# Kernel tuning notes

Hardware: AMD Instinct MI355X
Metric: run time of the kernel (lower is better)

## Reference

```python
import jax, jax.numpy as jnp
import numpy as np

NUM_USERS = 50000
NUM_ITEMS = 50000
N_NODES = NUM_USERS + NUM_ITEMS
NNZ = 3200000
EMB_DIM = 64
N_LAYERS = 3
BATCH = 16384


def setup_inputs() -> dict:
    key = jax.random.key(0)
    ks = jax.random.split(key, 7)
    user_emb = 0.1 * jax.random.normal(ks[0], (NUM_USERS, EMB_DIM), dtype=jnp.float32)
    item_emb = 0.1 * jax.random.normal(ks[1], (NUM_ITEMS, EMB_DIM), dtype=jnp.float32)
    edge_val = jax.random.uniform(ks[2], (NNZ,), dtype=jnp.float32)
    edge_src = jax.random.randint(ks[3], (NNZ,), 0, N_NODES, dtype=jnp.int32)
    edge_dst = jax.random.randint(ks[4], (NNZ,), 0, N_NODES, dtype=jnp.int32)
    users = jax.random.randint(ks[5], (BATCH,), 0, NUM_USERS, dtype=jnp.int32)
    items = jax.random.randint(ks[6], (BATCH,), 0, NUM_ITEMS, dtype=jnp.int32)
    return {"user_emb": user_emb, "item_emb": item_emb, "edge_val": edge_val,
            "edge_src": edge_src, "edge_dst": edge_dst, "users": users, "items": items}


def _computer(user_emb, item_emb, edge_val, edge_src, edge_dst):
    # LightGCN propagation: all_emb <- A @ all_emb, mean over layer outputs (incl. layer 0)
    all_emb = jnp.concatenate([user_emb, item_emb], axis=0)  # [N, D]
    acc = all_emb
    for _ in range(N_LAYERS):
        msg = edge_val[:, None] * all_emb[edge_src]          # [nnz, D]
        all_emb = jax.ops.segment_sum(msg, edge_dst, num_segments=N_NODES)
        acc = acc + all_emb
    light_out = acc / jnp.float32(N_LAYERS + 1)
    return light_out[:NUM_USERS], light_out[NUM_USERS:]


def reference(user_emb, item_emb, edge_val, edge_src, edge_dst, users, items):
    all_users, all_items = _computer(user_emb, item_emb, edge_val, edge_src, edge_dst)
    users_emb = all_users[users]                              # [B, D]
    items_emb = all_items[items]                              # [B, D]
    gamma = jnp.sum(users_emb * items_emb, axis=1)            # [B]
    return gamma
```

## Files before the change

### kernel.cpp

```cpp
#include <hip/hip_runtime.h>

#define NUM_USERS 50000
#define NUM_ITEMS 50000
#define N_NODES   100000
#define NNZ       3200000
#define EMB_DIM   64
#define N_LAYERS  3
#define BATCH     16384

#define NBUCK 512
#define ABITS 8
#define NODES_PER_BUCK 256
#define TILE_EDGES 8192
#define NBUCK_USED ((N_NODES + NODES_PER_BUCK - 1) / NODES_PER_BUCK)
#define CAP 9472
#define NCELL 1024

typedef unsigned long long ull;
typedef float v2f __attribute__((ext_vector_type(2)));

__device__ inline unsigned bf16pair(float a, float b) {
    unsigned ua = __float_as_uint(a), ub = __float_as_uint(b);
    unsigned r0 = (ua + 0x7fffu + ((ua >> 16) & 1u)) >> 16;
    unsigned r1 = (ub + 0x7fffu + ((ub >> 16) & 1u)) >> 16;
    return r0 | (r1 << 16);
}
__device__ inline float blo(unsigned u) { return __uint_as_float(u << 16); }
__device__ inline float bhi(unsigned u) { return __uint_as_float(u & 0xffff0000u); }

__device__ inline void pkfma(v2f& d, v2f a, v2f b) {
    asm("v_pk_fma_f32 %0, %1, %2, %0" : "+v"(d) : "v"(a), "v"(b));
}

__device__ inline void accP(v2f& sA, v2f& sB, v2f& sC, v2f& sD, uint4 g, unsigned r) {
    float w = (float)(r >> 17);
    v2f w2 = {w, w};
    v2f e0 = {blo(g.x), bhi(g.x)};
    v2f e1 = {blo(g.y), bhi(g.y)};
    v2f e2 = {blo(g.z), bhi(g.z)};
    v2f e3 = {blo(g.w), bhi(g.w)};
    pkfma(sA, e0, w2);
    pkfma(sB, e1, w2);
    pkfma(sC, e2, w2);
    pkfma(sD, e3, w2);
}

__device__ inline uint4 gath(const unsigned char* __restrict__ base, unsigned r, unsigned dOff) {
    unsigned off = ((r & 0x1FFFFu) << 7) + dOff;
    return *(const uint4*)(base + off);
}

__device__ inline void roundU(const unsigned char* __restrict__ A16,
                              const unsigned* __restrict__ p, unsigned dOff,
                              v2f& sA, v2f& sB, v2f& sC, v2f& sD) {
    uint4 R = *(const uint4*)p;
    uint4 g0 = gath(A16, R.x, dOff);
    uint4 g1 = gath(A16, R.y, dOff);
    uint4 g2 = gath(A16, R.z, dOff);
    uint4 g3 = gath(A16, R.w, dOff);
    accP(sA, sB, sC, sD, g0, R.x);
    accP(sA, sB, sC, sD, g1, R.y);
    accP(sA, sB, sC, sD, g2, R.z);
    accP(sA, sB, sC, sD, g3, R.w);
}

__device__ inline void pull_pair(const unsigned char* __restrict__ A16,
                                 uint4* __restrict__ B16,
                                 const unsigned* __restrict__ sorted,
                                 const int* __restrict__ rowStart,
                                 const int* __restrict__ deg,
                                 int nA, int nB, int d8, unsigned dOff) {
    int dA = deg[nA], dB = deg[nB];
    const unsigned* pA = sorted + rowStart[nA];
    const unsigned* pB = sorted + rowStart[nB];

    v2f s00 = {0.f,0.f}, s01 = {0.f,0.f}, s02 = {0.f,0.f}, s03 = {0.f,0.f};
    v2f s10 = {0.f,0.f}, s11 = {0.f,0.f}, s12 = {0.f,0.f}, s13 = {0.f,0.f};

    #pragma unroll
    for (int base = 0; base < 48; base += 4) {
        if (dA > base) roundU(A16, pA + base, dOff, s00, s01, s02, s03);
        if (dB > base) roundU(A16, pB + base, dOff, s10, s11, s12, s13);
    }
    if (__builtin_expect((dA > 48) || (dB > 48), 0)) {
        for (int base = 48; base < dA; base += 4)
            roundU(A16, pA + base, dOff, s00, s01, s02, s03);
        for (int base = 48; base < dB; base += 4)
            roundU(A16, pB + base, dOff, s10, s11, s12, s13);
    }

    const float k15 = 1.f / 32768.f;
    uint4 h;
    h.x = bf16pair(s00.x * k15, s00.y * k15);
    h.y = bf16pair(s01.x * k15, s01.y * k15);
    h.z = bf16pair(s02.x * k15, s02.y * k15);
    h.w = bf16pair(s03.x * k15, s03.y * k15);
    B16[(((long long)nA) << 3) + d8] = h;
    h.x = bf16pair(s10.x * k15, s10.y * k15);
    h.y = bf16pair(s11.x * k15, s11.y * k15);
    h.z = bf16pair(s12.x * k15, s12.y * k15);
    h.w = bf16pair(s13.x * k15, s13.y * k15);
    B16[(((long long)nB) << 3) + d8] = h;
}

__global__ void init_emb_kernel(const float* __restrict__ ue,
                                const float* __restrict__ ie,
                                unsigned* __restrict__ E0,
                                int* __restrict__ bucketCursor) {
    int idx = blockIdx.x * blockDim.x + threadIdx.x;
    if (blockIdx.x == 0 && threadIdx.x < 256) {
        bucketCursor[threadIdx.x]       = threadIdx.x * CAP;
        bucketCursor[threadIdx.x + 256] = (threadIdx.x + 256) * CAP;
    }
    const int total = N_NODES * (EMB_DIM / 4);
    if (idx >= total) return;
    const int uoff = NUM_USERS * (EMB_DIM / 4);
    float4 v;
    if (idx < uoff) v = ((const float4*)ue)[idx];
    else            v = ((const float4*)ie)[idx - uoff];
    uint2 h;
    h.x = bf16pair(v.x, v.y);
    h.y = bf16pair(v.z, v.w);
    ((uint2*)E0)[idx] = h;
}

__global__ void partA_kernel(const float* __restrict__ ev,
                             const int*  __restrict__ es,
                             const int*  __restrict__ ed,
                             int* __restrict__ bucketCursor,
                             ull* __restrict__ tmp) {
    __shared__ int hist[NBUCK];
    __shared__ int base[NBUCK];
    __shared__ int cnt2[NBUCK];
    int tid = threadIdx.x;
    int e0 = blockIdx.x * TILE_EDGES;

    int      mySrc[8], myDst[8];
    unsigned myQ[8];

    for (int i = tid; i < NBUCK; i += 1024) hist[i] = 0;
    __syncthreads();

    #pragma unroll
    for (int k = 0; k < 8; ++k) {
        int e = e0 + k * 1024 + tid;
        if (e < NNZ) {
            mySrc[k] = es[e];
            myDst[k] = ed[e];
            myQ[k]   = (unsigned)fminf(ev[e] * 32768.f + 0.5f, 32767.f);
            atomicAdd(&hist[((unsigned)myDst[k]) >> ABITS], 1);
        } else {
            myDst[k] = -1;
        }
    }
    __syncthreads();

    for (int i = tid; i < NBUCK; i += 1024) {
        int c = hist[i];
        base[i] = c ? atomicAdd(&bucketCursor[i], c) : 0;
        cnt2[i] = 0;
    }
    __syncthreads();

    #pragma unroll
    for (int k = 0; k < 8; ++k) {
        int dst = myDst[k];
        if (dst < 0) continue;
        int b = ((unsigned)dst) >> ABITS;
        int pos = base[b] + atomicAdd(&cnt2[b], 1);
        if (pos < (b + 1) * CAP) {
            ull rec = (ull)(unsigned)(mySrc[k] | ((dst & (NODES_PER_BUCK - 1)) << 17))
                    | ((ull)myQ[k] << 25);
            tmp[pos] = rec;
        }
    }
}

__global__ void partB_kernel(const ull* __restrict__ tmp,
                             const int* __restrict__ bucketCursor,
                             int* __restrict__ rowStart,
                             int* __restrict__ deg,
                             unsigned* __restrict__ sorted) {
    __shared__ int cnt[NCELL];
    __shared__ int nsc[NODES_PER_BUCK];
    __shared__ int nstart[NODES_PER_BUCK];
    __shared__ int cur[NCELL];
    int b = blockIdx.x;
    int tid = threadIdx.x;
    int nodeLo = b << ABITS;
    int startE = b * CAP;
    int endE   = bucketCursor[b];

    cnt[tid] = 0;
    __syncthreads();

    ull myRec[9];
    int myCell[9];
    int nRec = 0;
    #pragma unroll
    for (int k = 0; k < 9; ++k) {
        int i = startE + k * 1024 + tid;
        if (i < endE) {
            myRec[k] = tmp[i];
            nRec = k + 1;
            unsigned src = (unsigned)(myRec[k] & 0x1FFFFULL);
            int q = (int)(src >> 15); if (q > 3) q = 3;
            int dl = (int)((myRec[k] >> 17) & (NODES_PER_BUCK - 1));
            myCell[k] = (dl << 2) + q;
            atomicAdd(&cnt[myCell[k]], 1);
        }
    }
    __syncthreads();

    int p4 = 0;
    if (tid < NODES_PER_BUCK) {
        int tot = cnt[tid*4] + cnt[tid*4+1] + cnt[tid*4+2] + cnt[tid*4+3];
        p4 = (tot + 3) & ~3;
        nsc[tid] = p4;
    }
    __syncthreads();
    for (int o = 1; o < NODES_PER_BUCK; o <<= 1) {
        int add = 0;
        if (tid < NODES_PER_BUCK && tid >= o) add = nsc[tid - o];
        __syncthreads();
        if (tid < NODES_PER_BUCK) nsc[tid] += add;
        __syncthreads();
    }
    if (tid < NODES_PER_BUCK) {
        int ns = startE + nsc[tid] - p4;
        nstart[tid] = ns;
        int node = nodeLo + tid;
        if (node < N_NODES) {
            rowStart[node] = ns;
            deg[node] = p4;
        }
    }
    __syncthreads();

    {
        int n = tid >> 2, q = tid & 3;
        int c = nstart[n];
        if (q > 0) c += cnt[n*4];
        if (q > 1) c += cnt[n*4+1];
        if (q > 2) c += cnt[n*4+2];
        cur[tid] = c;
    }
    __syncthreads();

    for (int k = 0; k < nRec; ++k) {
        ull rec = myRec[k];
        unsigned o = (unsigned)(rec & 0x1FFFFULL) | ((unsigned)((rec >> 25) & 0x7FFF) << 17);
        int pos = atomicAdd(&cur[myCell[k]], 1);
        if (pos < startE + CAP) sorted[pos] = o;
    }
    __syncthreads();

    if (tid < NODES_PER_BUCK) {
        int tot = cnt[tid*4] + cnt[tid*4+1] + cnt[tid*4+2] + cnt[tid*4+3];
        int end = nstart[tid] + ((tot + 3) & ~3);
        for (int p = nstart[tid] + tot; p < end; ++p)
            if (p < startE + CAP) sorted[p] = 0;
    }
}

__global__ void __launch_bounds__(256, 6)
pull_sync_kernel(const unsigned char* __restrict__ A16,
                 uint4* __restrict__ B16,
                 const unsigned* __restrict__ sorted,
                 const int* __restrict__ rowStart,
                 const int* __restrict__ deg) {
    int wid = (blockIdx.x << 2) + (threadIdx.x >> 6);
    if (wid >= N_NODES / 16) return;
    int lane = threadIdx.x & 63;
    int eg = lane >> 3;
    int d8 = lane & 7;
    unsigned dOff = (unsigned)d8 << 4;
    int nA = (wid << 4) + (eg << 1);
    pull_pair(A16, B16, sorted, rowStart, deg, nA, nA + 1, d8, dOff);
}

__global__ void __launch_bounds__(256, 6)
pull_gated_kernel(const unsigned char* __restrict__ A16,
                  uint4* __restrict__ B16,
                  const unsigned* __restrict__ sorted,
                  const int* __restrict__ rowStart,
                  const int* __restrict__ deg,
                  const int* __restrict__ users,
                  const int* __restrict__ items) {
    int wid = (blockIdx.x << 2) + (threadIdx.x >> 6);
    if (wid >= (2 * BATCH) / 16) return;
    int lane = threadIdx.x & 63;
    int eg = lane >> 3;
    int d8 = lane & 7;
    unsigned dOff = (unsigned)d8 << 4;
    int e = (wid << 4) + (eg << 1);
    int nA = (e     < BATCH) ? users[e]     : NUM_USERS + items[e - BATCH];
    int nB = (e + 1 < BATCH) ? users[e + 1] : NUM_USERS + items[e + 1 - BATCH];
    pull_pair(A16, B16, sorted, rowStart, deg, nA, nB, d8, dOff);
}

__global__ void dot_kernel(const unsigned* __restrict__ E0,
                           const unsigned* __restrict__ B1,
                           const unsigned* __restrict__ B2,
                           const unsigned* __restrict__ B3,
                           const int* __restrict__ users,
                           const int* __restrict__ items,
                           float* __restrict__ out) {
    int t = blockIdx.x * blockDim.x + threadIdx.x;
    int b = t >> 5;
    int lane = t & 31;
    if (b >= BATCH) return;
    long long uo = ((long long)users[b] << 5) + lane;
    long long io = ((long long)(items[b] + NUM_USERS) << 5) + lane;
    unsigned a0 = E0[uo], a1 = B1[uo], a2 = B2[uo], a3 = B3[uo];
    unsigned c0 = E0[io], c1 = B1[io], c2 = B2[io], c3 = B3[io];
    float ux = (blo(a0) + blo(a1)) + (blo(a2) + blo(a3));
    float uy = (bhi(a0) + bhi(a1)) + (bhi(a2) + bhi(a3));
    float ix = (blo(c0) + blo(c1)) + (blo(c2) + blo(c3));
    float iy = (bhi(c0) + bhi(c1)) + (bhi(c2) + bhi(c3));
    float p = ux * ix + uy * iy;
    #pragma unroll
    for (int off = 16; off >= 1; off >>= 1)
        p += __shfl_xor(p, off, 64);
    if (lane == 0) out[b] = p * 0.0625f;
}

extern "C" void kernel_launch(void* const* d_in, const int* in_sizes, int n_in,
                              void* d_out, int out_size, void* d_ws, size_t ws_size,
                              hipStream_t stream) {
    const float* user_emb = (const float*)d_in[0];
    const float* item_emb = (const float*)d_in[1];
    const float* edge_val = (const float*)d_in[2];
    const int*   edge_src = (const int*)d_in[3];
    const int*   edge_dst = (const int*)d_in[4];
    const int*   users    = (const int*)d_in[5];
    const int*   items    = (const int*)d_in[6];
    float* out = (float*)d_out;

    const size_t emb16Bytes = (size_t)N_NODES * EMB_DIM * 2;
    const size_t sortBytes  = (size_t)NBUCK_USED * CAP * sizeof(unsigned);
    const size_t tmpBytes   = (size_t)NBUCK_USED * CAP * sizeof(ull);
    const size_t nodeBytes  = (size_t)N_NODES * sizeof(int);

    char* w = (char*)d_ws;
    unsigned* E0           = (unsigned*)(w); w += emb16Bytes;
    unsigned* B1           = (unsigned*)(w); w += emb16Bytes;
    unsigned* B2           = (unsigned*)(w); w += emb16Bytes;
    unsigned* B3           = (unsigned*)(w); w += emb16Bytes;
    unsigned* sorted       = (unsigned*)(w); w += sortBytes;
    ull*      tmp          = (ull*)(w);      w += tmpBytes;
    int*      deg          = (int*)(w);      w += nodeBytes;
    int*      rowStart     = (int*)(w);      w += nodeBytes;
    int*      bucketCursor = (int*)(w);      w += NBUCK * sizeof(int);

    const int vecTotal   = N_NODES * (EMB_DIM / 4);
    const int initBlocks = (vecTotal + 255) / 256;
    const int tileBlocks = (NNZ + TILE_EDGES - 1) / TILE_EDGES;

    init_emb_kernel<<<initBlocks, 256, 0, stream>>>(user_emb, item_emb, E0, bucketCursor);

    partA_kernel<<<tileBlocks, 1024, 0, stream>>>(edge_val, edge_src, edge_dst,
                                                  bucketCursor, tmp);
    partB_kernel<<<NBUCK_USED, 1024, 0, stream>>>(tmp, bucketCursor,
                                                  rowStart, deg, sorted);

    const int syncBlocks = (N_NODES / 16 + 3) / 4;
    pull_sync_kernel<<<syncBlocks, 256, 0, stream>>>((const unsigned char*)E0, (uint4*)B1,
                                                     sorted, rowStart, deg);
    pull_sync_kernel<<<syncBlocks, 256, 0, stream>>>((const unsigned char*)B1, (uint4*)B2,
                                                     sorted, rowStart, deg);

    const int gatedBlocks = ((2 * BATCH) / 16 + 3) / 4;
    pull_gated_kernel<<<gatedBlocks, 256, 0, stream>>>((const unsigned char*)B2, (uint4*)B3,
                                                       sorted, rowStart, deg, users, items);

    const int dotBlocks = (BATCH * 32 + 255) / 256;
    dot_kernel<<<dotBlocks, 256, 0, stream>>>(E0, B1, B2, B3, users, items, out);
}
```

Baseline: 296.0 us.

## Assign one wavefront per node in pull kernels with cross-lane reduction

Each pull kernel now gives a whole 64-lane wavefront to a single destination node instead of 16 nodes per wavefront (two per 8-lane group). The 8 edge groups split that node's edge list, and the partial sums are combined with xor shuffles before one group writes the bf16 row. Edge indices are read and results written with nontemporal hints. The aim is better load balance and more memory-level parallelism across the ~32 edges per node, at the cost of shuffle reductions, padding tails, and 8x more wavefronts.

Measured after the change: 279.5 us. 1.06x faster.

```diff
diff --git a/kernel.cpp b/kernel.cpp
--- a/kernel.cpp
+++ b/kernel.cpp
@@ -18,6 +18,7 @@
 
 typedef unsigned long long ull;
 typedef float v2f __attribute__((ext_vector_type(2)));
+typedef unsigned v4u __attribute__((ext_vector_type(4)));
 
 __device__ inline unsigned bf16pair(float a, float b) {
     unsigned ua = __float_as_uint(a), ub = __float_as_uint(b);
@@ -30,6 +31,9 @@
 
 __device__ inline void pkfma(v2f& d, v2f a, v2f b) {
     asm("v_pk_fma_f32 %0, %1, %2, %0" : "+v"(d) : "v"(a), "v"(b));
+}
+__device__ inline void pkadd(v2f& d, v2f a) {
+    asm("v_pk_add_f32 %0, %1, %0" : "+v"(d) : "v"(a));
 }
 
 __device__ inline void accP(v2f& sA, v2f& sB, v2f& sC, v2f& sD, uint4 g, unsigned r) {
@@ -50,57 +54,71 @@
     return *(const uint4*)(base + off);
 }
 
-__device__ inline void roundU(const unsigned char* __restrict__ A16,
-                              const unsigned* __restrict__ p, unsigned dOff,
-                              v2f& sA, v2f& sB, v2f& sC, v2f& sD) {
-    uint4 R = *(const uint4*)p;
-    uint4 g0 = gath(A16, R.x, dOff);
-    uint4 g1 = gath(A16, R.y, dOff);
-    uint4 g2 = gath(A16, R.z, dOff);
-    uint4 g3 = gath(A16, R.w, dOff);
-    accP(sA, sB, sC, sD, g0, R.x);
-    accP(sA, sB, sC, sD, g1, R.y);
-    accP(sA, sB, sC, sD, g2, R.z);
-    accP(sA, sB, sC, sD, g3, R.w);
-}
-
-__device__ inline void pull_pair(const unsigned char* __restrict__ A16,
-                                 uint4* __restrict__ B16,
+__device__ inline unsigned ntl(const unsigned* __restrict__ p) {
+    return __builtin_nontemporal_load(p);
+}
+
+__device__ inline void wred(v2f& s) {
+    v2f t;
+    t.x = __shfl_xor(s.x, 8, 64);  t.y = __shfl_xor(s.y, 8, 64);  pkadd(s, t);
+    t.x = __shfl_xor(s.x, 16, 64); t.y = __shfl_xor(s.y, 16, 64); pkadd(s, t);
+    t.x = __shfl_xor(s.x, 32, 64); t.y = __shfl_xor(s.y, 32, 64); pkadd(s, t);
+}
+
+__device__ inline void pull_node(const unsigned char* __restrict__ A16,
+                                 unsigned* __restrict__ B16,
                                  const unsigned* __restrict__ sorted,
-                                 const int* __restrict__ rowStart,
-                                 const int* __restrict__ deg,
-                                 int nA, int nB, int d8, unsigned dOff) {
-    int dA = deg[nA], dB = deg[nB];
-    const unsigned* pA = sorted + rowStart[nA];
-    const unsigned* pB = sorted + rowStart[nB];
-
-    v2f s00 = {0.f,0.f}, s01 = {0.f,0.f}, s02 = {0.f,0.f}, s03 = {0.f,0.f};
-    v2f s10 = {0.f,0.f}, s11 = {0.f,0.f}, s12 = {0.f,0.f}, s13 = {0.f,0.f};
-
-    #pragma unroll
-    for (int base = 0; base < 48; base += 4) {
-        if (dA > base) roundU(A16, pA + base, dOff, s00, s01, s02, s03);
-        if (dB > base) roundU(A16, pB + base, dOff, s10, s11, s12, s13);
-    }
-    if (__builtin_expect((dA > 48) || (dB > 48), 0)) {
-        for (int base = 48; base < dA; base += 4)
-            roundU(A16, pA + base, dOff, s00, s01, s02, s03);
-        for (int base = 48; base < dB; base += 4)
-            roundU(A16, pB + base, dOff, s10, s11, s12, s13);
-    }
-
-    const float k15 = 1.f / 32768.f;
-    uint4 h;
-    h.x = bf16pair(s00.x * k15, s00.y * k15);
-    h.y = bf16pair(s01.x * k15, s01.y * k15);
-    h.z = bf16pair(s02.x * k15, s02.y * k15);
-    h.w = bf16pair(s03.x * k15, s03.y * k15);
-    B16[(((long long)nA) << 3) + d8] = h;
-    h.x = bf16pair(s10.x * k15, s10.y * k15);
-    h.y = bf16pair(s11.x * k15, s11.y * k15);
-    h.z = bf16pair(s12.x * k15, s12.y * k15);
-    h.w = bf16pair(s13.x * k15, s13.y * k15);
-    B16[(((long long)nB) << 3) + d8] = h;
+                                 int node, int start, int cnt, int lane) {
+    int eg = lane >> 3;
+    int d8 = lane & 7;
+    unsigned dOff = (unsigned)d8 << 4;
+    const unsigned* ep = sorted + start;
+
+    v2f sA = {0.f,0.f}, sB = {0.f,0.f}, sC = {0.f,0.f}, sD = {0.f,0.f};
+    int j = 0;
+    while (j + 32 <= cnt) {
+        unsigned r0 = ntl(ep + j + eg),      r1 = ntl(ep + j + 8 + eg);
+        unsigned r2 = ntl(ep + j + 16 + eg), r3 = ntl(ep + j + 24 + eg);
+        uint4 g0 = gath(A16, r0, dOff);
+        uint4 g1 = gath(A16, r1, dOff);
+        uint4 g2 = gath(A16, r2, dOff);
+        uint4 g3 = gath(A16, r3, dOff);
+        accP(sA, sB, sC, sD, g0, r0);
+        accP(sA, sB, sC, sD, g1, r1);
+        accP(sA, sB, sC, sD, g2, r2);
+        accP(sA, sB, sC, sD, g3, r3);
+        j += 32;
+    }
+    if (j + 16 <= cnt) {
+        unsigned r0 = ntl(ep + j + eg), r1 = ntl(ep + j + 8 + eg);
+        uint4 g0 = gath(A16, r0, dOff);
+        uint4 g1 = gath(A16, r1, dOff);
+        accP(sA, sB, sC, sD, g0, r0);
+        accP(sA, sB, sC, sD, g1, r1);
+        j += 16;
+    }
+    if (j < cnt) {
+        int i0 = j + eg, i1 = j + 8 + eg;
+        unsigned r0 = (i0 < cnt) ? ntl(ep + i0) : 0u;
+        unsigned r1 = (i1 < cnt) ? ntl(ep + i1) : 0u;
+        uint4 g0 = gath(A16, r0, dOff);
+        uint4 g1 = gath(A16, r1, dOff);
+        accP(sA, sB, sC, sD, g0, r0);
+        accP(sA, sB, sC, sD, g1, r1);
+    }
+
+    wred(sA); wred(sB); wred(sC); wred(sD);
+
+    if (eg == 0) {
+        const float k15 = 1.f / 32768.f;
+        v4u h;
+        h.x = bf16pair(sA.x * k15, sA.y * k15);
+        h.y = bf16pair(sB.x * k15, sB.y * k15);
+        h.z = bf16pair(sC.x * k15, sC.y * k15);
+        h.w = bf16pair(sD.x * k15, sD.y * k15);
+        v4u* dst = (v4u*)(B16 + (((long long)node) << 5) + ((long long)d8 << 2));
+        __builtin_nontemporal_store(h, dst);
+    }
 }
 
 __global__ void init_emb_kernel(const float* __restrict__ ue,
@@ -263,40 +281,34 @@
     }
 }
 
-__global__ void __launch_bounds__(256, 6)
-pull_sync_kernel(const unsigned char* __restrict__ A16,
-                 uint4* __restrict__ B16,
-                 const unsigned* __restrict__ sorted,
-                 const int* __restrict__ rowStart,
-                 const int* __restrict__ deg) {
-    int wid = (blockIdx.x << 2) + (threadIdx.x >> 6);
-    if (wid >= N_NODES / 16) return;
-    int lane = threadIdx.x & 63;
-    int eg = lane >> 3;
-    int d8 = lane & 7;
-    unsigned dOff = (unsigned)d8 << 4;
-    int nA = (wid << 4) + (eg << 1);
-    pull_pair(A16, B16, sorted, rowStart, deg, nA, nA + 1, d8, dOff);
-}
-
-__global__ void __launch_bounds__(256, 6)
-pull_gated_kernel(const unsigned char* __restrict__ A16,
-                  uint4* __restrict__ B16,
-                  const unsigned* __restrict__ sorted,
-                  const int* __restrict__ rowStart,
-                  const int* __restrict__ deg,
-                  const int* __restrict__ users,
-                  const int* __restrict__ items) {
-    int wid = (blockIdx.x << 2) + (threadIdx.x >> 6);
-    if (wid >= (2 * BATCH) / 16) return;
-    int lane = threadIdx.x & 63;
-    int eg = lane >> 3;
-    int d8 = lane & 7;
-    unsigned dOff = (unsigned)d8 << 4;
-    int e = (wid << 4) + (eg << 1);
-    int nA = (e     < BATCH) ? users[e]     : NUM_USERS + items[e - BATCH];
-    int nB = (e + 1 < BATCH) ? users[e + 1] : NUM_USERS + items[e + 1 - BATCH];
-    pull_pair(A16, B16, sorted, rowStart, deg, nA, nB, d8, dOff);
+__global__ void pull_sync_kernel(const unsigned char* __restrict__ A16,
+                                 unsigned* __restrict__ B16,
+                                 const unsigned* __restrict__ sorted,
+                                 const int* __restrict__ rowStart,
+                                 const int* __restrict__ deg) {
+    int t = blockIdx.x * blockDim.x + threadIdx.x;
+    int node = __builtin_amdgcn_readfirstlane(t >> 6);
+    if (node >= N_NODES) return;
+    int start = rowStart[node];
+    int cnt   = deg[node];
+    pull_node(A16, B16, sorted, node, start, cnt, t & 63);
+}
+
+__global__ void pull_gated_kernel(const unsigned char* __restrict__ A16,
+                                  unsigned* __restrict__ B16,
+                                  const unsigned* __restrict__ sorted,
+                                  const int* __restrict__ rowStart,
+                                  const int* __restrict__ deg,
+                                  const int* __restrict__ users,
+                                  const int* __restrict__ items) {
+    int t = blockIdx.x * blockDim.x + threadIdx.x;
+    int e = __builtin_amdgcn_readfirstlane(t >> 6);
+    if (e >= 2 * BATCH) return;
+    int node = (e < BATCH) ? users[e] : (NUM_USERS + items[e - BATCH]);
+    node = __builtin_amdgcn_readfirstlane(node);
+    int start = rowStart[node];
+    int cnt   = deg[node];
+    pull_node(A16, B16, sorted, node, start, cnt, t & 63);
 }
 
 __global__ void dot_kernel(const unsigned* __restrict__ E0,
@@ -364,14 +376,14 @@
     partB_kernel<<<NBUCK_USED, 1024, 0, stream>>>(tmp, bucketCursor,
                                                   rowStart, deg, sorted);
 
-    const int syncBlocks = (N_NODES / 16 + 3) / 4;
-    pull_sync_kernel<<<syncBlocks, 256, 0, stream>>>((const unsigned char*)E0, (uint4*)B1,
+    const int pullBlocks = (N_NODES * 64 + 255) / 256;
+    pull_sync_kernel<<<pullBlocks, 256, 0, stream>>>((const unsigned char*)E0, B1,
                                                      sorted, rowStart, deg);
-    pull_sync_kernel<<<syncBlocks, 256, 0, stream>>>((const unsigned char*)B1, (uint4*)B2,
+    pull_sync_kernel<<<pullBlocks, 256, 0, stream>>>((const unsigned char*)B1, B2,
                                                      sorted, rowStart, deg);
 
-    const int gatedBlocks = ((2 * BATCH) / 16 + 3) / 4;
-    pull_gated_kernel<<<gatedBlocks, 256, 0, stream>>>((const unsigned char*)B2, (uint4*)B3,
+    const int gatedBlocks = (2 * BATCH * 64 + 255) / 256;
+    pull_gated_kernel<<<gatedBlocks, 256, 0, stream>>>((const unsigned char*)B2, B3,
                                                        sorted, rowStart, deg, users, items);
 
     const int dotBlocks = (BATCH * 32 + 255) / 256;
```
